# Kernel tuning notes

Measured on AMD Instinct MI355X. Metric: run time of the kernel, lower is better.

Reference implementation:

```python
import jax, jax.numpy as jnp
import numpy as np

B, L, D = 2, 256, 256  # batch, length, raw feature dim (W dims are D+1)

def setup_inputs() -> dict:
    key = jax.random.key(0)
    k1, k2, k3, kw = jax.random.split(key, 4)
    layer1 = jax.random.normal(k1, (B, L, D), dtype=jnp.float32)
    layer2 = jax.random.normal(k2, (B, L, D), dtype=jnp.float32)
    layer3 = jax.random.normal(k3, (B, L, D), dtype=jnp.float32)
    # xavier_normal_ for a 3D tensor: fan_in = D+1 * (D+1) receptive? torch treats
    # dim0 as fan_out-ish; we just use a matched-scale gaussian (correctness of the
    # contraction math is what matters for the kernel baseline).
    std = float(np.sqrt(2.0 / ((D + 1) + (D + 1) * (D + 1))))
    W = jax.random.normal(kw, (D + 1, D + 1, D + 1), dtype=jnp.float32) * std
    return {"layer1": layer1, "layer2": layer2, "layer3": layer3, "W": W}

def _append_ones(x):
    ones = jnp.ones(x.shape[:2] + (1,), dtype=x.dtype)
    return jnp.concatenate([x, ones], axis=-1)

def reference(layer1, layer2, layer3, W):
    l1 = _append_ones(layer1)  # [n, L, a]
    l2 = _append_ones(layer2)  # [n, L, b]
    l3 = _append_ones(layer3)  # [n, L, c]
    # Chained contraction: nia,abc -> nibc ; nibc,njb -> nijc ; nijc,nkc -> nijk
    t = jnp.einsum('nia,abc->nibc', l1, W)
    t = jnp.einsum('nibc,njb->nijc', t, l2)
    out = jnp.einsum('nijc,nkc->nijk', t, l3)
    return out
```

## Files before the change

kernel.cpp:

```cpp
#include <hip/hip_runtime.h>

typedef unsigned short u16;
typedef __attribute__((ext_vector_type(8))) short bf16x8;
typedef __attribute__((ext_vector_type(4))) float f32x4;

#define GLOAD_LDS16(gsrc, ldst)                                               \
  __builtin_amdgcn_global_load_lds(                                           \
      (const __attribute__((address_space(1))) void*)(gsrc),                  \
      (__attribute__((address_space(3))) void*)(ldst), 16, 0, 0)

#define LDSOFF(p) \
  ((unsigned)(uintptr_t)(__attribute__((address_space(3))) const void*)(p))

__device__ __forceinline__ u16 f2bf(float x) {
  unsigned u = __float_as_uint(x);
  u = (u + 0x7FFFu + ((u >> 16) & 1u)) >> 16;
  return (u16)u;
}

__global__ void prep_l_kernel(const float* __restrict__ l1,
                              const float* __restrict__ l2,
                              const float* __restrict__ l3,
                              u16* __restrict__ o1, u16* __restrict__ o2,
                              u16* __restrict__ o3) {
  int idx = blockIdx.x * 256 + threadIdx.x;
  const int NR = 512 * 288;
  if (idx >= 3 * NR) return;
  int which = idx / NR, rem = idx - which * NR;
  int r = rem / 288, p = rem - r * 288;
  const float* s = which == 0 ? l1 : which == 1 ? l2 : l3;
  u16* d = which == 0 ? o1 : which == 1 ? o2 : o3;
  float v = (p < 256) ? s[r * 256 + p] : (p == 256 ? 1.0f : 0.0f);
  d[rem] = f2bf(v);
}

__global__ void prep_w_kernel(const float* __restrict__ W, u16* __restrict__ W2) {
  __shared__ float tile[32][33];
  const int a0 = blockIdx.x * 32, c0 = blockIdx.y * 32, b = blockIdx.z;
  const int t = threadIdx.x;
#pragma unroll
  for (int p = 0; p < 4; ++p) {
    int idx = t + p * 256;
    int cl = idx & 31, r = idx >> 5;
    int a = a0 + r, c = c0 + cl;
    float v = 0.0f;
    if (a < 257 && b < 257 && c < 257) v = W[((long)a * 257 + b) * 257 + c];
    tile[r][cl] = v;
  }
  __syncthreads();
#pragma unroll
  for (int p = 0; p < 4; ++p) {
    int idx = t + p * 256;
    int al = idx & 31, ccl = idx >> 5;
    W2[((long)(c0 + ccl) * 288 + b) * 288 + (a0 + al)] = f2bf(tile[al][ccl]);
  }
}

__global__ __launch_bounds__(256) void gemm_nt(
    const u16* __restrict__ A, const u16* __restrict__ B, u16* __restrict__ C,
    int K, int lda, int ldb, int ldc) {
  __shared__ u16 As[128 * 64];
  __shared__ u16 Bs[128 * 64];
  const int t = threadIdx.x;
  const int bid = blockIdx.x;
  const int xcd = bid & 7, s = bid >> 3;
  const int nt = xcd * 81 + (s >> 2);
  const int mt = s & 3;
  const int m0 = mt * 128, n0 = nt * 128;
  const int lane = t & 63;
  const int w = t >> 6;
  const int wr = (w >> 1) * 64, wc = (w & 1) * 64;
  const int r16 = lane & 15;
  const int cgrp = lane >> 4;
  const int rr = cgrp * 4;

  const u16* PA = A + (long)m0 * lda;
  const u16* PB = B + (long)n0 * ldb;

#define STG64(P, ld, dst, k0)                                                 \
  {                                                                           \
    _Pragma("unroll") for (int _p = 0; _p < 4; ++_p) {                        \
      int _q = t + _p * 256;                                                  \
      int _r = _q >> 3, _g = (_q & 7) ^ (_r & 7);                             \
      GLOAD_LDS16(P + (long)_r * (ld) + (k0) + _g * 8, &dst[_q * 8]);         \
    }                                                                         \
  }
#define STG64T(P, ld, dst, k0)                                                \
  {                                                                           \
    _Pragma("unroll") for (int _p = 0; _p < 4; ++_p) {                        \
      int _q = t + _p * 256;                                                  \
      int _r = _q >> 3, _g = (_q & 7) ^ (_r & 7);                             \
      if (_g < 4)                                                             \
        GLOAD_LDS16(P + (long)_r * (ld) + (k0) + _g * 8, &dst[_q * 8]);       \
    }                                                                         \
  }

  f32x4 acc[4][4];
  const f32x4 zero = {0.f, 0.f, 0.f, 0.f};
#pragma unroll
  for (int i = 0; i < 4; ++i)
#pragma unroll
    for (int j = 0; j < 4; ++j) acc[i][j] = zero;

#pragma unroll
  for (int ks = 0; ks < 5; ++ks) {
    const int k0 = ks * 64;
    if (ks < 4) {
      STG64(PA, lda, As, k0);
      STG64(PB, ldb, Bs, k0);
    } else {
      STG64T(PA, lda, As, k0);
      STG64T(PB, ldb, Bs, k0);
    }
    __syncthreads();
    const int nkk = (ks < 4) ? 2 : 1;
#pragma unroll
    for (int kk = 0; kk < 2; ++kk) {
      if (kk < nkk) {
        bf16x8 af[4], bfr[4];
#pragma unroll
        for (int mi = 0; mi < 4; ++mi) {
          int R = wr + mi * 16 + r16;
          af[mi] = *(const bf16x8*)(&As[R * 64 + (((kk * 4 + cgrp) ^ (R & 7)) * 8)]);
        }
#pragma unroll
        for (int ni = 0; ni < 4; ++ni) {
          int R = wc + ni * 16 + r16;
          bfr[ni] = *(const bf16x8*)(&Bs[R * 64 + (((kk * 4 + cgrp) ^ (R & 7)) * 8)]);
        }
#pragma unroll
        for (int mi = 0; mi < 4; ++mi)
#pragma unroll
          for (int ni = 0; ni < 4; ++ni)
            acc[mi][ni] = __builtin_amdgcn_mfma_f32_16x16x32_bf16(
                af[mi], bfr[ni], acc[mi][ni], 0, 0, 0);
      }
    }
    __syncthreads();
  }
#undef STG64
#undef STG64T

#pragma unroll
  for (int mi = 0; mi < 4; ++mi) {
    int gm = m0 + wr + mi * 16 + rr;
#pragma unroll
    for (int ni = 0; ni < 4; ++ni) {
      int gc = n0 + wc + ni * 16 + r16;
#pragma unroll
      for (int r = 0; r < 4; ++r)
        C[(long)(gm + r) * ldc + gc] = f2bf(acc[mi][ni][r]);
    }
  }
}

__global__ __launch_bounds__(512, 2) void fused23(
    const u16* __restrict__ l2b, const u16* __restrict__ l3b,
    const u16* __restrict__ T1, float* __restrict__ out) {
  __shared__ u16 S[128 * 296];
  __shared__ u16 Bst[4][288 * 32];
  const int t = threadIdx.x;
  const int lane = t & 63;
  const int w = t >> 6;

  const int bid = blockIdx.x;
  const int xcd = bid & 7;
  const int seq = bid >> 3;
  const int ni = xcd * 64 + (seq >> 1);
  const int half = seq & 1;
  const int n = ni >> 8;

  const int r16 = lane & 15;
  const int cgrp = lane >> 4;
  const int kb = cgrp * 8;
  const int rr = cgrp * 4;
  const f32x4 zero = {0.f, 0.f, 0.f, 0.f};

  const u16* A2 = l2b + (long)n * 73728 + (long)(half * 128) * 288;
  const u16* BT = T1 + (long)ni * 82944;
  const u16* B3 = l3b + (long)n * 73728;
  const unsigned BOF = LDSOFF(&Bst[0][0]);

#define ISSUE_A(buf, kk)                                                      \
  {                                                                           \
    int q1 = w * 144 + lane;                                                  \
    int r1 = q1 >> 2, g1 = (q1 & 3) ^ ((r1 >> 2) & 3);                        \
    GLOAD_LDS16(BT + (long)r1 * 288 + (kk) * 32 + g1 * 8, &Bst[(buf)][q1 * 8]); \
    int q2 = q1 + 64;                                                         \
    int r2 = q2 >> 2, g2 = (q2 & 3) ^ ((r2 >> 2) & 3);                        \
    GLOAD_LDS16(BT + (long)r2 * 288 + (kk) * 32 + g2 * 8, &Bst[(buf)][q2 * 8]); \
    if (lane < 16) {                                                          \
      int q3 = w * 144 + 128 + lane;                                          \
      int r3 = q3 >> 2, g3 = (q3 & 3) ^ ((r3 >> 2) & 3);                      \
      GLOAD_LDS16(BT + (long)r3 * 288 + (kk) * 32 + g3 * 8, &Bst[(buf)][q3 * 8]); \
    }                                                                         \
  }
#define ISSUE_B(buf, kk)                                                      \
  {                                                                           \
    int q1 = w * 128 + lane;                                                  \
    int r1 = q1 >> 2, g1 = (q1 & 3) ^ ((r1 >> 2) & 3);                        \
    GLOAD_LDS16(B3 + (long)r1 * 288 + (kk) * 32 + g1 * 8, &Bst[(buf)][q1 * 8]); \
    int q2 = q1 + 64;                                                         \
    int r2 = q2 >> 2, g2 = (q2 & 3) ^ ((r2 >> 2) & 3);                        \
    GLOAD_LDS16(B3 + (long)r2 * 288 + (kk) * 32 + g2 * 8, &Bst[(buf)][q2 * 8]); \
  }

  {
    const int wm = w & 3, wn = w >> 2;
    f32x4 acc[2][9];
#pragma unroll
    for (int i = 0; i < 2; ++i)
#pragma unroll
      for (int j = 0; j < 9; ++j) acc[i][j] = zero;

    bf16x8 afr[18];
#pragma unroll
    for (int k = 0; k < 9; ++k)
#pragma unroll
      for (int mi = 0; mi < 2; ++mi)
        afr[k * 2 + mi] = *(const bf16x8*)(A2 +
            (long)(wm * 32 + mi * 16 + r16) * 288 + k * 32 + kb);

    ISSUE_A(0, 0);
    ISSUE_A(1, 1);

#define FA_STEP(K, NW)                                                        \
  {                                                                           \
    if ((K) + 2 <= 8) ISSUE_A(((K) + 2) & 3, (K) + 2);                        \
    asm volatile("s_waitcnt vmcnt(" #NW ")" ::: "memory");                    \
    __builtin_amdgcn_sched_barrier(0);                                        \
    __builtin_amdgcn_s_barrier();                                             \
    __builtin_amdgcn_sched_barrier(0);                                        \
    bf16x8 bf[9];                                                             \
    _Pragma("unroll") for (int nj = 0; nj < 9; ++nj) {                        \
      const int R = wn * 144 + nj * 16 + r16;                                 \
      unsigned ao = BOF + (unsigned)((((K) & 3) * 9216 + R * 32 +             \
                                      ((cgrp ^ ((R >> 2) & 3)) * 8)) * 2);    \
      asm volatile("ds_read_b128 %0, %1" : "=v"(bf[nj]) : "v"(ao));           \
    }                                                                         \
    asm volatile("s_waitcnt lgkmcnt(0)" ::: "memory");                        \
    __builtin_amdgcn_sched_barrier(0);                                        \
    _Pragma("unroll") for (int nj = 0; nj < 9; ++nj) {                        \
      acc[0][nj] = __builtin_amdgcn_mfma_f32_16x16x32_bf16(                   \
          afr[(K) * 2 + 0], bf[nj], acc[0][nj], 0, 0, 0);                     \
      acc[1][nj] = __builtin_amdgcn_mfma_f32_16x16x32_bf16(                   \
          afr[(K) * 2 + 1], bf[nj], acc[1][nj], 0, 0, 0);                     \
    }                                                                         \
  }
    FA_STEP(0, 6) FA_STEP(1, 6) FA_STEP(2, 6) FA_STEP(3, 6) FA_STEP(4, 6)
    FA_STEP(5, 6) FA_STEP(6, 6) FA_STEP(7, 3) FA_STEP(8, 0)
#undef FA_STEP

    __syncthreads();
    ISSUE_B(0, 0);
    ISSUE_B(1, 1);
#pragma unroll
    for (int mi = 0; mi < 2; ++mi)
#pragma unroll
      for (int nj = 0; nj < 9; ++nj)
#pragma unroll
        for (int q = 0; q < 4; ++q)
          S[(wm * 32 + mi * 16 + rr + q) * 296 + wn * 144 + nj * 16 + r16] =
              f2bf(acc[mi][nj][q]);
  }
  __syncthreads();

  {
    const int wm = w & 1, wn = w >> 1;
    f32x4 acc[4][4];
#pragma unroll
    for (int i = 0; i < 4; ++i)
#pragma unroll
      for (int j = 0; j < 4; ++j) acc[i][j] = zero;

#define FB_STEP(K, NW)                                                        \
  {                                                                           \
    if ((K) + 2 <= 8) ISSUE_B(((K) + 2) & 3, (K) + 2);                        \
    asm volatile("s_waitcnt vmcnt(" #NW ")" ::: "memory");                    \
    __builtin_amdgcn_sched_barrier(0);                                        \
    __builtin_amdgcn_s_barrier();                                             \
    __builtin_amdgcn_sched_barrier(0);                                        \
    bf16x8 bf[4];                                                             \
    _Pragma("unroll") for (int nj = 0; nj < 4; ++nj) {                        \
      const int R = wn * 64 + nj * 16 + r16;                                  \
      unsigned ao = BOF + (unsigned)((((K) & 3) * 9216 + R * 32 +             \
                                      ((cgrp ^ ((R >> 2) & 3)) * 8)) * 2);    \
      asm volatile("ds_read_b128 %0, %1" : "=v"(bf[nj]) : "v"(ao));           \
    }                                                                         \
    asm volatile("s_waitcnt lgkmcnt(0)" ::: "memory");                        \
    __builtin_amdgcn_sched_barrier(0);                                        \
    bf16x8 af[4];                                                             \
    _Pragma("unroll") for (int mi = 0; mi < 4; ++mi)                          \
      af[mi] = *(const bf16x8*)(&S[(wm * 64 + mi * 16 + r16) * 296 +          \
                                   (K) * 32 + kb]);                           \
    _Pragma("unroll") for (int nj = 0; nj < 4; ++nj)                          \
      _Pragma("unroll") for (int mi = 0; mi < 4; ++mi)                        \
        acc[mi][nj] = __builtin_amdgcn_mfma_f32_16x16x32_bf16(                \
            af[mi], bf[nj], acc[mi][nj], 0, 0, 0);                            \
  }
    FB_STEP(0, 4) FB_STEP(1, 4) FB_STEP(2, 4) FB_STEP(3, 4) FB_STEP(4, 4)
    FB_STEP(5, 4) FB_STEP(6, 4) FB_STEP(7, 2) FB_STEP(8, 0)
#undef FB_STEP

    float* O = out + (long)ni * 65536 + (long)(half * 128 + wm * 64) * 256 + wn * 64;
#pragma unroll
    for (int mi = 0; mi < 4; ++mi)
#pragma unroll
      for (int nj = 0; nj < 4; ++nj)
#pragma unroll
        for (int q = 0; q < 4; ++q)
          O[(long)(mi * 16 + rr + q) * 256 + nj * 16 + r16] = acc[mi][nj][q];
  }
#undef ISSUE_A
#undef ISSUE_B
}

extern "C" void kernel_launch(void* const* d_in, const int* in_sizes, int n_in,
                              void* d_out, int out_size, void* d_ws, size_t ws_size,
                              hipStream_t stream) {
  const float* l1 = (const float*)d_in[0];
  const float* l2 = (const float*)d_in[1];
  const float* l3 = (const float*)d_in[2];
  const float* W = (const float*)d_in[3];
  float* out = (float*)d_out;
  char* ws = (char*)d_ws;

  const long LB = 512L * 288 * 2;
  u16* l1b = (u16*)ws;
  u16* l2b = (u16*)(ws + LB);
  u16* l3b = (u16*)(ws + 2 * LB);
  u16* T1 = (u16*)(ws + 3 * LB);
  u16* W2 = (u16*)d_out;

  prep_l_kernel<<<1728, 256, 0, stream>>>(l1, l2, l3, l1b, l2b, l3b);

  dim3 gw(9, 9, 288);
  prep_w_kernel<<<gw, 256, 0, stream>>>(W, W2);

  gemm_nt<<<2592, 256, 0, stream>>>(l1b, W2, T1, 288, 288, 288, 82944);

  fused23<<<1024, 512, 0, stream>>>(l2b, l3b, T1, out);
}
```

Before: 160.4 us.

## Double-buffer gemm_nt K-loop and interleave LDS reads with MFMA via partial waits

The first GEMM changes from single-buffered 64-wide K steps with two barriers each to double-buffered 32-wide K steps, prefetching the next tile while the current one computes. It also raises the occupancy hint and uses raw ds_read with staged lgkmcnt waits and s_setprio around MFMA groups. The fused kernel gets the same staged-wait and priority scheme, and its swizzle changes from (r>>2)&3 to (r>>1)&3. The goal is to hide global-to-LDS and LDS-read latency behind matrix math and reduce bank conflicts, at the cost of more barriers per K and hand-tuned wait counts that can break if instruction counts shift.

```diff
diff --git a/kernel.cpp b/kernel.cpp
--- a/kernel.cpp
+++ b/kernel.cpp
@@ -11,6 +11,8 @@
 
 #define LDSOFF(p) \
   ((unsigned)(uintptr_t)(__attribute__((address_space(3))) const void*)(p))
+
+#define SB0 __builtin_amdgcn_sched_barrier(0)
 
 __device__ __forceinline__ u16 f2bf(float x) {
   unsigned u = __float_as_uint(x);
@@ -56,16 +58,16 @@
   }
 }
 
-__global__ __launch_bounds__(256) void gemm_nt(
+__global__ __launch_bounds__(256, 4) void gemm_nt(
     const u16* __restrict__ A, const u16* __restrict__ B, u16* __restrict__ C,
     int K, int lda, int ldb, int ldc) {
-  __shared__ u16 As[128 * 64];
-  __shared__ u16 Bs[128 * 64];
+  __shared__ u16 As[2][4096];
+  __shared__ u16 Bs[2][4096];
   const int t = threadIdx.x;
   const int bid = blockIdx.x;
-  const int xcd = bid & 7, s = bid >> 3;
-  const int nt = xcd * 81 + (s >> 2);
-  const int mt = s & 3;
+  const int xcd = bid & 7, sq = bid >> 3;
+  const int nt = xcd * 81 + (sq >> 2);
+  const int mt = sq & 3;
   const int m0 = mt * 128, n0 = nt * 128;
   const int lane = t & 63;
   const int w = t >> 6;
@@ -73,25 +75,20 @@
   const int r16 = lane & 15;
   const int cgrp = lane >> 4;
   const int rr = cgrp * 4;
+  const unsigned ABase = LDSOFF(&As[0][0]);
+  const unsigned BBase = LDSOFF(&Bs[0][0]);
+  (void)K;
 
   const u16* PA = A + (long)m0 * lda;
   const u16* PB = B + (long)n0 * ldb;
 
-#define STG64(P, ld, dst, k0)                                                 \
-  {                                                                           \
-    _Pragma("unroll") for (int _p = 0; _p < 4; ++_p) {                        \
+#define STG(buf, k0)                                                          \
+  {                                                                           \
+    _Pragma("unroll") for (int _p = 0; _p < 2; ++_p) {                        \
       int _q = t + _p * 256;                                                  \
-      int _r = _q >> 3, _g = (_q & 7) ^ (_r & 7);                             \
-      GLOAD_LDS16(P + (long)_r * (ld) + (k0) + _g * 8, &dst[_q * 8]);         \
-    }                                                                         \
-  }
-#define STG64T(P, ld, dst, k0)                                                \
-  {                                                                           \
-    _Pragma("unroll") for (int _p = 0; _p < 4; ++_p) {                        \
-      int _q = t + _p * 256;                                                  \
-      int _r = _q >> 3, _g = (_q & 7) ^ (_r & 7);                             \
-      if (_g < 4)                                                             \
-        GLOAD_LDS16(P + (long)_r * (ld) + (k0) + _g * 8, &dst[_q * 8]);       \
+      int _r = _q >> 2, _g = (_q & 3) ^ ((_r >> 1) & 3);                      \
+      GLOAD_LDS16(PA + (long)_r * lda + (k0) + _g * 8, &As[buf][_q * 8]);     \
+      GLOAD_LDS16(PB + (long)_r * ldb + (k0) + _g * 8, &Bs[buf][_q * 8]);     \
     }                                                                         \
   }
 
@@ -102,44 +99,53 @@
 #pragma unroll
     for (int j = 0; j < 4; ++j) acc[i][j] = zero;
 
-#pragma unroll
-  for (int ks = 0; ks < 5; ++ks) {
-    const int k0 = ks * 64;
-    if (ks < 4) {
-      STG64(PA, lda, As, k0);
-      STG64(PB, ldb, Bs, k0);
-    } else {
-      STG64T(PA, lda, As, k0);
-      STG64T(PB, ldb, Bs, k0);
-    }
-    __syncthreads();
-    const int nkk = (ks < 4) ? 2 : 1;
-#pragma unroll
-    for (int kk = 0; kk < 2; ++kk) {
-      if (kk < nkk) {
-        bf16x8 af[4], bfr[4];
-#pragma unroll
-        for (int mi = 0; mi < 4; ++mi) {
-          int R = wr + mi * 16 + r16;
-          af[mi] = *(const bf16x8*)(&As[R * 64 + (((kk * 4 + cgrp) ^ (R & 7)) * 8)]);
-        }
-#pragma unroll
-        for (int ni = 0; ni < 4; ++ni) {
-          int R = wc + ni * 16 + r16;
-          bfr[ni] = *(const bf16x8*)(&Bs[R * 64 + (((kk * 4 + cgrp) ^ (R & 7)) * 8)]);
-        }
-#pragma unroll
-        for (int mi = 0; mi < 4; ++mi)
-#pragma unroll
-          for (int ni = 0; ni < 4; ++ni)
-            acc[mi][ni] = __builtin_amdgcn_mfma_f32_16x16x32_bf16(
-                af[mi], bfr[ni], acc[mi][ni], 0, 0, 0);
-      }
-    }
-    __syncthreads();
-  }
-#undef STG64
-#undef STG64T
+  STG(0, 0);
+
+#define GCOL(NI)                                                              \
+  __builtin_amdgcn_s_setprio(1);                                              \
+  acc[0][NI] = __builtin_amdgcn_mfma_f32_16x16x32_bf16(af[0], bf[NI], acc[0][NI], 0, 0, 0); \
+  acc[1][NI] = __builtin_amdgcn_mfma_f32_16x16x32_bf16(af[1], bf[NI], acc[1][NI], 0, 0, 0); \
+  acc[2][NI] = __builtin_amdgcn_mfma_f32_16x16x32_bf16(af[2], bf[NI], acc[2][NI], 0, 0, 0); \
+  acc[3][NI] = __builtin_amdgcn_mfma_f32_16x16x32_bf16(af[3], bf[NI], acc[3][NI], 0, 0, 0); \
+  __builtin_amdgcn_s_setprio(0);                                              \
+  SB0;
+
+#define GSTEP(KS, NW)                                                         \
+  {                                                                           \
+    if ((KS) < 8) STG(((KS) + 1) & 1, ((KS) + 1) * 32);                       \
+    asm volatile("s_waitcnt vmcnt(" #NW ")" ::: "memory");                    \
+    SB0;                                                                      \
+    __builtin_amdgcn_s_barrier();                                             \
+    SB0;                                                                      \
+    bf16x8 af[4], bf[4];                                                      \
+    _Pragma("unroll") for (int mi = 0; mi < 4; ++mi) {                        \
+      int R = wr + mi * 16 + r16;                                             \
+      unsigned ao = ABase + (unsigned)(((((KS) & 1) * 4096) + R * 32 +        \
+                                       ((cgrp ^ ((R >> 1) & 3)) * 8)) * 2);   \
+      asm volatile("ds_read_b128 %0, %1" : "=v"(af[mi]) : "v"(ao));           \
+    }                                                                         \
+    _Pragma("unroll") for (int ni = 0; ni < 4; ++ni) {                        \
+      int R = wc + ni * 16 + r16;                                             \
+      unsigned ao = BBase + (unsigned)(((((KS) & 1) * 4096) + R * 32 +        \
+                                       ((cgrp ^ ((R >> 1) & 3)) * 8)) * 2);   \
+      asm volatile("ds_read_b128 %0, %1" : "=v"(bf[ni]) : "v"(ao));           \
+    }                                                                         \
+    SB0;                                                                      \
+    asm volatile("s_waitcnt lgkmcnt(3)" ::: "memory"); SB0;                   \
+    GCOL(0)                                                                   \
+    asm volatile("s_waitcnt lgkmcnt(2)" ::: "memory"); SB0;                   \
+    GCOL(1)                                                                   \
+    asm volatile("s_waitcnt lgkmcnt(1)" ::: "memory"); SB0;                   \
+    GCOL(2)                                                                   \
+    asm volatile("s_waitcnt lgkmcnt(0)" ::: "memory"); SB0;                   \
+    GCOL(3)                                                                   \
+  }
+
+  GSTEP(0, 4) GSTEP(1, 4) GSTEP(2, 4) GSTEP(3, 4) GSTEP(4, 4)
+  GSTEP(5, 4) GSTEP(6, 4) GSTEP(7, 4) GSTEP(8, 0)
+#undef GSTEP
+#undef GCOL
+#undef STG
 
 #pragma unroll
   for (int mi = 0; mi < 4; ++mi) {
@@ -180,28 +186,29 @@
   const u16* BT = T1 + (long)ni * 82944;
   const u16* B3 = l3b + (long)n * 73728;
   const unsigned BOF = LDSOFF(&Bst[0][0]);
+  const unsigned SOF = LDSOFF(&S[0]);
 
 #define ISSUE_A(buf, kk)                                                      \
   {                                                                           \
     int q1 = w * 144 + lane;                                                  \
-    int r1 = q1 >> 2, g1 = (q1 & 3) ^ ((r1 >> 2) & 3);                        \
+    int r1 = q1 >> 2, g1 = (q1 & 3) ^ ((r1 >> 1) & 3);                        \
     GLOAD_LDS16(BT + (long)r1 * 288 + (kk) * 32 + g1 * 8, &Bst[(buf)][q1 * 8]); \
     int q2 = q1 + 64;                                                         \
-    int r2 = q2 >> 2, g2 = (q2 & 3) ^ ((r2 >> 2) & 3);                        \
+    int r2 = q2 >> 2, g2 = (q2 & 3) ^ ((r2 >> 1) & 3);                        \
     GLOAD_LDS16(BT + (long)r2 * 288 + (kk) * 32 + g2 * 8, &Bst[(buf)][q2 * 8]); \
     if (lane < 16) {                                                          \
       int q3 = w * 144 + 128 + lane;                                          \
-      int r3 = q3 >> 2, g3 = (q3 & 3) ^ ((r3 >> 2) & 3);                      \
+      int r3 = q3 >> 2, g3 = (q3 & 3) ^ ((r3 >> 1) & 3);                      \
       GLOAD_LDS16(BT + (long)r3 * 288 + (kk) * 32 + g3 * 8, &Bst[(buf)][q3 * 8]); \
     }                                                                         \
   }
 #define ISSUE_B(buf, kk)                                                      \
   {                                                                           \
     int q1 = w * 128 + lane;                                                  \
-    int r1 = q1 >> 2, g1 = (q1 & 3) ^ ((r1 >> 2) & 3);                        \
+    int r1 = q1 >> 2, g1 = (q1 & 3) ^ ((r1 >> 1) & 3);                        \
     GLOAD_LDS16(B3 + (long)r1 * 288 + (kk) * 32 + g1 * 8, &Bst[(buf)][q1 * 8]); \
     int q2 = q1 + 64;                                                         \
-    int r2 = q2 >> 2, g2 = (q2 & 3) ^ ((r2 >> 2) & 3);                        \
+    int r2 = q2 >> 2, g2 = (q2 & 3) ^ ((r2 >> 1) & 3);                        \
     GLOAD_LDS16(B3 + (long)r2 * 288 + (kk) * 32 + g2 * 8, &Bst[(buf)][q2 * 8]); \
   }
 
@@ -220,36 +227,44 @@
       for (int mi = 0; mi < 2; ++mi)
         afr[k * 2 + mi] = *(const bf16x8*)(A2 +
             (long)(wm * 32 + mi * 16 + r16) * 288 + k * 32 + kb);
+    SB0;
 
     ISSUE_A(0, 0);
     ISSUE_A(1, 1);
 
+#define FA_MM(NJ)                                                             \
+  __builtin_amdgcn_s_setprio(1);                                              \
+  acc[0][NJ] = __builtin_amdgcn_mfma_f32_16x16x32_bf16(afc0, bf[NJ], acc[0][NJ], 0, 0, 0); \
+  acc[1][NJ] = __builtin_amdgcn_mfma_f32_16x16x32_bf16(afc1, bf[NJ], acc[1][NJ], 0, 0, 0); \
+  __builtin_amdgcn_s_setprio(0);
+
 #define FA_STEP(K, NW)                                                        \
   {                                                                           \
     if ((K) + 2 <= 8) ISSUE_A(((K) + 2) & 3, (K) + 2);                        \
     asm volatile("s_waitcnt vmcnt(" #NW ")" ::: "memory");                    \
-    __builtin_amdgcn_sched_barrier(0);                                        \
+    SB0;                                                                      \
     __builtin_amdgcn_s_barrier();                                             \
-    __builtin_amdgcn_sched_barrier(0);                                        \
+    SB0;                                                                      \
     bf16x8 bf[9];                                                             \
     _Pragma("unroll") for (int nj = 0; nj < 9; ++nj) {                        \
       const int R = wn * 144 + nj * 16 + r16;                                 \
       unsigned ao = BOF + (unsigned)((((K) & 3) * 9216 + R * 32 +             \
-                                      ((cgrp ^ ((R >> 2) & 3)) * 8)) * 2);    \
+                                      ((cgrp ^ ((R >> 1) & 3)) * 8)) * 2);    \
       asm volatile("ds_read_b128 %0, %1" : "=v"(bf[nj]) : "v"(ao));           \
     }                                                                         \
-    asm volatile("s_waitcnt lgkmcnt(0)" ::: "memory");                        \
-    __builtin_amdgcn_sched_barrier(0);                                        \
-    _Pragma("unroll") for (int nj = 0; nj < 9; ++nj) {                        \
-      acc[0][nj] = __builtin_amdgcn_mfma_f32_16x16x32_bf16(                   \
-          afr[(K) * 2 + 0], bf[nj], acc[0][nj], 0, 0, 0);                     \
-      acc[1][nj] = __builtin_amdgcn_mfma_f32_16x16x32_bf16(                   \
-          afr[(K) * 2 + 1], bf[nj], acc[1][nj], 0, 0, 0);                     \
-    }                                                                         \
+    SB0;                                                                      \
+    const bf16x8 afc0 = afr[(K) * 2 + 0], afc1 = afr[(K) * 2 + 1];            \
+    asm volatile("s_waitcnt lgkmcnt(6)" ::: "memory"); SB0;                   \
+    FA_MM(0) FA_MM(1) FA_MM(2) SB0;                                           \
+    asm volatile("s_waitcnt lgkmcnt(3)" ::: "memory"); SB0;                   \
+    FA_MM(3) FA_MM(4) FA_MM(5) SB0;                                           \
+    asm volatile("s_waitcnt lgkmcnt(0)" ::: "memory"); SB0;                   \
+    FA_MM(6) FA_MM(7) FA_MM(8) SB0;                                           \
   }
     FA_STEP(0, 6) FA_STEP(1, 6) FA_STEP(2, 6) FA_STEP(3, 6) FA_STEP(4, 6)
     FA_STEP(5, 6) FA_STEP(6, 6) FA_STEP(7, 3) FA_STEP(8, 0)
 #undef FA_STEP
+#undef FA_MM
 
     __syncthreads();
     ISSUE_B(0, 0);
@@ -273,34 +288,48 @@
 #pragma unroll
       for (int j = 0; j < 4; ++j) acc[i][j] = zero;
 
+#define FB_MM(NI)                                                             \
+  __builtin_amdgcn_s_setprio(1);                                              \
+  acc[0][NI] = __builtin_amdgcn_mfma_f32_16x16x32_bf16(af[0], bf[NI], acc[0][NI], 0, 0, 0); \
+  acc[1][NI] = __builtin_amdgcn_mfma_f32_16x16x32_bf16(af[1], bf[NI], acc[1][NI], 0, 0, 0); \
+  acc[2][NI] = __builtin_amdgcn_mfma_f32_16x16x32_bf16(af[2], bf[NI], acc[2][NI], 0, 0, 0); \
+  acc[3][NI] = __builtin_amdgcn_mfma_f32_16x16x32_bf16(af[3], bf[NI], acc[3][NI], 0, 0, 0); \
+  __builtin_amdgcn_s_setprio(0);                                              \
+  SB0;
+
 #define FB_STEP(K, NW)                                                        \
   {                                                                           \
     if ((K) + 2 <= 8) ISSUE_B(((K) + 2) & 3, (K) + 2);                        \
     asm volatile("s_waitcnt vmcnt(" #NW ")" ::: "memory");                    \
-    __builtin_amdgcn_sched_barrier(0);                                        \
+    SB0;                                                                      \
     __builtin_amdgcn_s_barrier();                                             \
-    __builtin_amdgcn_sched_barrier(0);                                        \
-    bf16x8 bf[4];                                                             \
+    SB0;                                                                      \
+    bf16x8 af[4], bf[4];                                                      \
+    _Pragma("unroll") for (int mi = 0; mi < 4; ++mi) {                        \
+      unsigned ao = SOF + (unsigned)(((wm * 64 + mi * 16 + r16) * 296 +       \
+                                      (K) * 32 + kb) * 2);                    \
+      asm volatile("ds_read_b128 %0, %1" : "=v"(af[mi]) : "v"(ao));           \
+    }                                                                         \
     _Pragma("unroll") for (int nj = 0; nj < 4; ++nj) {                        \
       const int R = wn * 64 + nj * 16 + r16;                                  \
       unsigned ao = BOF + (unsigned)((((K) & 3) * 9216 + R * 32 +             \
-                                      ((cgrp ^ ((R >> 2) & 3)) * 8)) * 2);    \
+                                      ((cgrp ^ ((R >> 1) & 3)) * 8)) * 2);    \
       asm volatile("ds_read_b128 %0, %1" : "=v"(bf[nj]) : "v"(ao));           \
     }                                                                         \
-    asm volatile("s_waitcnt lgkmcnt(0)" ::: "memory");                        \
-    __builtin_amdgcn_sched_barrier(0);                                        \
-    bf16x8 af[4];                                                             \
-    _Pragma("unroll") for (int mi = 0; mi < 4; ++mi)                          \
-      af[mi] = *(const bf16x8*)(&S[(wm * 64 + mi * 16 + r16) * 296 +          \
-                                   (K) * 32 + kb]);                           \
-    _Pragma("unroll") for (int nj = 0; nj < 4; ++nj)                          \
-      _Pragma("unroll") for (int mi = 0; mi < 4; ++mi)                        \
-        acc[mi][nj] = __builtin_amdgcn_mfma_f32_16x16x32_bf16(                \
-            af[mi], bf[nj], acc[mi][nj], 0, 0, 0);                            \
+    SB0;                                                                      \
+    asm volatile("s_waitcnt lgkmcnt(3)" ::: "memory"); SB0;                   \
+    FB_MM(0)                                                                  \
+    asm volatile("s_waitcnt lgkmcnt(2)" ::: "memory"); SB0;                   \
+    FB_MM(1)                                                                  \
+    asm volatile("s_waitcnt lgkmcnt(1)" ::: "memory"); SB0;                   \
+    FB_MM(2)                                                                  \
+    asm volatile("s_waitcnt lgkmcnt(0)" ::: "memory"); SB0;                   \
+    FB_MM(3)                                                                  \
   }
     FB_STEP(0, 4) FB_STEP(1, 4) FB_STEP(2, 4) FB_STEP(3, 4) FB_STEP(4, 4)
     FB_STEP(5, 4) FB_STEP(6, 4) FB_STEP(7, 2) FB_STEP(8, 0)
 #undef FB_STEP
+#undef FB_MM
 
     float* O = out + (long)ni * 65536 + (long)(half * 128 + wm * 64) * 256 + wn * 64;
 #pragma unroll
```

After: 159.1 us. About the same (-0.8%).
